# Performance work log

Measured on AMD Instinct MI355X. Metric: run time of the kernel, lower is better.

## Reference

```python
import jax, jax.numpy as jnp
import numpy as np

B = 524288   # batch
I = 12       # input_props
R = 6        # output_props (rules)
J = 2        # templates per rule
L = 2        # feature width
V = 4        # variables


def setup_inputs() -> dict:
    key = jax.random.key(0)
    ks = jax.random.split(key, 7)
    concrete_features = jax.random.uniform(ks[0], (B, I, L), dtype=jnp.float32)
    templates = jax.random.uniform(ks[1], (R, J, L), dtype=jnp.float32)           # U(0,1)
    gammas = jax.random.uniform(ks[2], (R, J, L), dtype=jnp.float32) * 0.4 + 0.4  # U(0.4,0.8)
    body_W = jax.random.normal(ks[3], (R, J, V, L), dtype=jnp.float32) * 0.5
    body_b = jax.random.normal(ks[4], (R, J, V), dtype=jnp.float32) * 0.1
    head_W = jax.random.normal(ks[5], (R, L, V), dtype=jnp.float32) * 0.5
    head_b = jax.random.normal(ks[6], (R, L), dtype=jnp.float32) * 0.1
    return {"concrete_features": concrete_features, "templates": templates,
            "gammas": gammas, "body_W": body_W, "body_b": body_b,
            "head_W": head_W, "head_b": head_b}


def reference(concrete_features, templates, gammas, body_W, body_b, head_W, head_b):
    # "sigmoid" in the original is clamp(x, 0, 1)
    g = jnp.clip(gammas, 0.0, 1.0)            # [R,J,L]
    w = 1.0 - g                               # per-dim match weight
    # match_scores[b,r,j,i] = sum_l w[r,j,l] * (templates[r,j,l] - f[b,i,l])^2
    # expand the square to avoid materializing a [B,R,J,I,L] tensor
    c0 = jnp.sum(w * templates * templates, axis=-1)                       # [R,J]
    cross = jnp.einsum('rjl,bil->brji', w * templates, concrete_features)  # [B,R,J,I]
    quad = jnp.einsum('rjl,bil->brji', w, concrete_features ** 2)          # [B,R,J,I]
    match_scores = c0[None, :, :, None] - 2.0 * cross + quad               # [B,R,J,I]
    attn = jax.nn.softmax(-match_scores, axis=-1)                          # over input_props
    # soft-selected feature per (rule, template): [B,R,J,L]
    selected = jnp.einsum('brji,bil->brjl', attn, concrete_features)
    # body Linear per (r,j), then sum over j (biases also sum over j)
    captured = jnp.einsum('brjl,rjvl->brv', selected, body_W) + jnp.sum(body_b, axis=1)  # [B,R,V]
    # head Linear per rule
    out = jnp.einsum('brv,rlv->brl', captured, head_W) + head_b            # [B,R,L]
    return out
```

## Files before the change

### kernel.cpp

```cpp
#include <hip/hip_runtime.h>

#define NI 12
#define NR 6
#define NJ 2
#define NL 2
#define NV 4

typedef float v2f __attribute__((ext_vector_type(2)));


__global__ __launch_bounds__(256) void
abstraction_fused(const float* __restrict__ feat,
                  const float* __restrict__ templates,
                  const float* __restrict__ gammas,
                  const float* __restrict__ body_W,
                  const float* __restrict__ body_b,
                  const float* __restrict__ head_W,
                  const float* __restrict__ head_b,
                  float* __restrict__ out, int B) {
    __shared__ float sG[NR * NJ * 5];
    __shared__ float sM[NR * NL * NJ * NL];
    __shared__ float sC[NR * NL];

    const int t = threadIdx.x;
    const float LOG2E = 1.4426950408889634f;

    if (t < NR * NJ) {
        const int g = t;
        float g0 = fminf(fmaxf(gammas[g * NL + 0], 0.f), 1.f);
        float g1 = fminf(fmaxf(gammas[g * NL + 1], 0.f), 1.f);
        float w0 = 1.f - g0, w1 = 1.f - g1;
        float t0 = templates[g * NL + 0], t1 = templates[g * NL + 1];
        float wt0 = w0 * t0, wt1 = w1 * t1;
        float c0 = wt0 * t0 + wt1 * t1;
        sG[g * 5 + 0] = 2.f * LOG2E * wt0;
        sG[g * 5 + 1] = 2.f * LOG2E * wt1;
        sG[g * 5 + 2] = -LOG2E * w0;
        sG[g * 5 + 3] = -LOG2E * w1;
        sG[g * 5 + 4] = -LOG2E * c0;
    } else if (t >= 64 && t < 64 + NR * NL) {
        const int idx = t - 64;
        const int r = idx >> 1, l = idx & 1;
        float acc = head_b[r * NL + l];
        #pragma unroll
        for (int v = 0; v < NV; ++v) {
            float bs = body_b[(r * NJ + 0) * NV + v] + body_b[(r * NJ + 1) * NV + v];
            acc = fmaf(head_W[(r * NL + l) * NV + v], bs, acc);
        }
        sC[idx] = acc;
    } else if (t >= 128 && t < 128 + NR * NL * NJ * NL) {
        const int idx = t - 128;
        const int lp = idx & 1, j = (idx >> 1) & 1, l = (idx >> 2) & 1, r = idx >> 3;
        float acc = 0.f;
        #pragma unroll
        for (int v = 0; v < NV; ++v)
            acc = fmaf(head_W[(r * NL + l) * NV + v],
                       body_W[((r * NJ + j) * NV + v) * NL + lp], acc);
        sM[idx] = acc;
    }
    __syncthreads();

    const int b = blockIdx.x * blockDim.x + t;
    if (b >= B) return;

    const float4* fp = (const float4*)(feat + (size_t)b * (NI * NL));
    float f0[NI], f1[NI];
    #pragma unroll
    for (int k = 0; k < 6; ++k) {
        float4 v = fp[k];
        f0[2 * k + 0] = v.x; f1[2 * k + 0] = v.y;
        f0[2 * k + 1] = v.z; f1[2 * k + 1] = v.w;
    }

    float o[NR * NL];
    #pragma unroll
    for (int r = 0; r < NR; ++r) {
        float o0 = sC[r * 2 + 0];
        float o1 = sC[r * 2 + 1];
        #pragma unroll
        for (int j = 0; j < NJ; ++j) {
            const int g = r * NJ + j;
            const v2f A0 = sG[g * 5 + 0];
            const v2f A1 = sG[g * 5 + 1];
            const v2f W0 = sG[g * 5 + 2];
            const v2f W1 = sG[g * 5 + 3];
            const v2f Cn = sG[g * 5 + 4];
            v2f den = 0.f, a0 = 0.f, a1 = 0.f;
            #pragma unroll
            for (int i = 0; i < NI; i += 2) {
                v2f X0 = { f0[i], f0[i + 1] };
                v2f X1 = { f1[i], f1[i + 1] };
                v2f n = __builtin_elementwise_fma(X0, __builtin_elementwise_fma(W0, X0, A0), Cn);
                n = __builtin_elementwise_fma(X1, __builtin_elementwise_fma(W1, X1, A1), n);
                v2f p = { __builtin_amdgcn_exp2f(n.x), __builtin_amdgcn_exp2f(n.y) };
                den += p;
                a0 = __builtin_elementwise_fma(p, X0, a0);
                a1 = __builtin_elementwise_fma(p, X1, a1);
            }
            float d = den.x + den.y;
            float rinv = __builtin_amdgcn_rcpf(d);
            float s0 = (a0.x + a0.y) * rinv;
            float s1 = (a1.x + a1.y) * rinv;
            const float m00 = sM[((r * 2 + 0) * 2 + j) * 2 + 0];
            const float m01 = sM[((r * 2 + 0) * 2 + j) * 2 + 1];
            const float m10 = sM[((r * 2 + 1) * 2 + j) * 2 + 0];
            const float m11 = sM[((r * 2 + 1) * 2 + j) * 2 + 1];
            o0 = fmaf(s0, m00, o0); o0 = fmaf(s1, m01, o0);
            o1 = fmaf(s0, m10, o1); o1 = fmaf(s1, m11, o1);
        }
        o[r * 2 + 0] = o0;
        o[r * 2 + 1] = o1;
    }

    float4* op = (float4*)(out + (size_t)b * (NR * NL));
    op[0] = make_float4(o[0], o[1], o[2], o[3]);
    op[1] = make_float4(o[4], o[5], o[6], o[7]);
    op[2] = make_float4(o[8], o[9], o[10], o[11]);
}

extern "C" void kernel_launch(void* const* d_in, const int* in_sizes, int n_in,
                              void* d_out, int out_size, void* d_ws, size_t ws_size,
                              hipStream_t stream) {
    (void)n_in; (void)out_size; (void)d_ws; (void)ws_size;
    const float* feat      = (const float*)d_in[0];
    const float* templates = (const float*)d_in[1];
    const float* gammas    = (const float*)d_in[2];
    const float* body_W    = (const float*)d_in[3];
    const float* body_b    = (const float*)d_in[4];
    const float* head_W    = (const float*)d_in[5];
    const float* head_b    = (const float*)d_in[6];
    float* out = (float*)d_out;

    int B = in_sizes[0] / (NI * NL);
    int blocks = (B + 255) / 256;
    hipLaunchKernelGGL(abstraction_fused, dim3(blocks), dim3(256), 0, stream,
                       feat, templates, gammas, body_W, body_b, head_W, head_b,
                       out, B);
}
```

Measured before the change: 107.7 us.

## Split parameter precompute into separate kernel reading constants from workspace

Moves the per-block parameter folding (templates/gammas/body/head weights) into a one-block precompute kernel that writes a packed record into the workspace. The main kernel then reads these uniform values straight from global memory, likely as scalar loads, with no shared memory and no __syncthreads. This removes redundant per-block setup work and the block-wide barrier. The cost is a second kernel launch and a dependency between the two kernels.

```diff
diff --git a/kernel.cpp b/kernel.cpp
--- a/kernel.cpp
+++ b/kernel.cpp
@@ -8,59 +8,63 @@
 
 typedef float v2f __attribute__((ext_vector_type(2)));
 
+#define LOG2E 1.4426950408889634f
 
-__global__ __launch_bounds__(256) void
-abstraction_fused(const float* __restrict__ feat,
-                  const float* __restrict__ templates,
-                  const float* __restrict__ gammas,
-                  const float* __restrict__ body_W,
-                  const float* __restrict__ body_b,
-                  const float* __restrict__ head_W,
-                  const float* __restrict__ head_b,
-                  float* __restrict__ out, int B) {
-    __shared__ float sG[NR * NJ * 5];
-    __shared__ float sM[NR * NL * NJ * NL];
-    __shared__ float sC[NR * NL];
 
+__global__ __launch_bounds__(64) void
+abstraction_params(const float* __restrict__ templates,
+                   const float* __restrict__ gammas,
+                   const float* __restrict__ body_W,
+                   const float* __restrict__ body_b,
+                   const float* __restrict__ head_W,
+                   const float* __restrict__ head_b,
+                   float* __restrict__ P) {
     const int t = threadIdx.x;
-    const float LOG2E = 1.4426950408889634f;
-
     if (t < NR * NJ) {
-        const int g = t;
+        const int g = t, r = g >> 1, j = g & 1;
         float g0 = fminf(fmaxf(gammas[g * NL + 0], 0.f), 1.f);
         float g1 = fminf(fmaxf(gammas[g * NL + 1], 0.f), 1.f);
         float w0 = 1.f - g0, w1 = 1.f - g1;
         float t0 = templates[g * NL + 0], t1 = templates[g * NL + 1];
-        float wt0 = w0 * t0, wt1 = w1 * t1;
-        float c0 = wt0 * t0 + wt1 * t1;
-        sG[g * 5 + 0] = 2.f * LOG2E * wt0;
-        sG[g * 5 + 1] = 2.f * LOG2E * wt1;
-        sG[g * 5 + 2] = -LOG2E * w0;
-        sG[g * 5 + 3] = -LOG2E * w1;
-        sG[g * 5 + 4] = -LOG2E * c0;
-    } else if (t >= 64 && t < 64 + NR * NL) {
-        const int idx = t - 64;
-        const int r = idx >> 1, l = idx & 1;
+        float A0 = 2.f * LOG2E * w0 * t0, A1 = 2.f * LOG2E * w1 * t1;
+        float W0 = -LOG2E * w0, W1 = -LOG2E * w1;
+        float Cn = -LOG2E * (w0 * t0 * t0 + w1 * t1 * t1);
+        float* rec = P + g * 16;
+        rec[0] = A0; rec[1] = A0;
+        rec[2] = A1; rec[3] = A1;
+        rec[4] = W0; rec[5] = W0;
+        rec[6] = W1; rec[7] = W1;
+        rec[8] = Cn; rec[9] = Cn;
+        #pragma unroll
+        for (int l = 0; l < NL; ++l) {
+            #pragma unroll
+            for (int lp = 0; lp < NL; ++lp) {
+                float acc = 0.f;
+                #pragma unroll
+                for (int v = 0; v < NV; ++v)
+                    acc = fmaf(head_W[(r * NL + l) * NV + v],
+                               body_W[((r * NJ + j) * NV + v) * NL + lp], acc);
+                rec[10 + l * 2 + lp] = acc;
+            }
+        }
+        rec[14] = 0.f; rec[15] = 0.f;
+    } else if (t >= 32 && t < 32 + NR * NL) {
+        const int idx = t - 32, r = idx >> 1, l = idx & 1;
         float acc = head_b[r * NL + l];
-        #pragma unroll
-        for (int v = 0; v < NV; ++v) {
-            float bs = body_b[(r * NJ + 0) * NV + v] + body_b[(r * NJ + 1) * NV + v];
-            acc = fmaf(head_W[(r * NL + l) * NV + v], bs, acc);
-        }
-        sC[idx] = acc;
-    } else if (t >= 128 && t < 128 + NR * NL * NJ * NL) {
-        const int idx = t - 128;
-        const int lp = idx & 1, j = (idx >> 1) & 1, l = (idx >> 2) & 1, r = idx >> 3;
-        float acc = 0.f;
         #pragma unroll
         for (int v = 0; v < NV; ++v)
             acc = fmaf(head_W[(r * NL + l) * NV + v],
-                       body_W[((r * NJ + j) * NV + v) * NL + lp], acc);
-        sM[idx] = acc;
+                       body_b[(r * NJ + 0) * NV + v] + body_b[(r * NJ + 1) * NV + v],
+                       acc);
+        P[192 + idx] = acc;
     }
-    __syncthreads();
+}
 
-    const int b = blockIdx.x * blockDim.x + t;
+__global__ __launch_bounds__(256) void
+abstraction_main(const float* __restrict__ feat,
+                 const float* __restrict__ P,
+                 float* __restrict__ out, int B) {
+    const int b = blockIdx.x * 256 + threadIdx.x;
     if (b >= B) return;
 
     const float4* fp = (const float4*)(feat + (size_t)b * (NI * NL));
@@ -75,16 +79,16 @@
     float o[NR * NL];
     #pragma unroll
     for (int r = 0; r < NR; ++r) {
-        float o0 = sC[r * 2 + 0];
-        float o1 = sC[r * 2 + 1];
+        float o0 = P[192 + r * 2 + 0];
+        float o1 = P[192 + r * 2 + 1];
         #pragma unroll
         for (int j = 0; j < NJ; ++j) {
-            const int g = r * NJ + j;
-            const v2f A0 = sG[g * 5 + 0];
-            const v2f A1 = sG[g * 5 + 1];
-            const v2f W0 = sG[g * 5 + 2];
-            const v2f W1 = sG[g * 5 + 3];
-            const v2f Cn = sG[g * 5 + 4];
+            const float* __restrict__ rec = P + (r * NJ + j) * 16;
+            const v2f A0 = *(const v2f*)(rec + 0);
+            const v2f A1 = *(const v2f*)(rec + 2);
+            const v2f W0 = *(const v2f*)(rec + 4);
+            const v2f W1 = *(const v2f*)(rec + 6);
+            const v2f Cn = *(const v2f*)(rec + 8);
             v2f den = 0.f, a0 = 0.f, a1 = 0.f;
             #pragma unroll
             for (int i = 0; i < NI; i += 2) {
@@ -101,12 +105,8 @@
             float rinv = __builtin_amdgcn_rcpf(d);
             float s0 = (a0.x + a0.y) * rinv;
             float s1 = (a1.x + a1.y) * rinv;
-            const float m00 = sM[((r * 2 + 0) * 2 + j) * 2 + 0];
-            const float m01 = sM[((r * 2 + 0) * 2 + j) * 2 + 1];
-            const float m10 = sM[((r * 2 + 1) * 2 + j) * 2 + 0];
-            const float m11 = sM[((r * 2 + 1) * 2 + j) * 2 + 1];
-            o0 = fmaf(s0, m00, o0); o0 = fmaf(s1, m01, o0);
-            o1 = fmaf(s0, m10, o1); o1 = fmaf(s1, m11, o1);
+            o0 = fmaf(s0, rec[10], o0); o0 = fmaf(s1, rec[11], o0);
+            o1 = fmaf(s0, rec[12], o1); o1 = fmaf(s1, rec[13], o1);
         }
         o[r * 2 + 0] = o0;
         o[r * 2 + 1] = o1;
@@ -121,7 +121,7 @@
 extern "C" void kernel_launch(void* const* d_in, const int* in_sizes, int n_in,
                               void* d_out, int out_size, void* d_ws, size_t ws_size,
                               hipStream_t stream) {
-    (void)n_in; (void)out_size; (void)d_ws; (void)ws_size;
+    (void)n_in; (void)out_size; (void)ws_size;
     const float* feat      = (const float*)d_in[0];
     const float* templates = (const float*)d_in[1];
     const float* gammas    = (const float*)d_in[2];
@@ -130,10 +130,13 @@
     const float* head_W    = (const float*)d_in[5];
     const float* head_b    = (const float*)d_in[6];
     float* out = (float*)d_out;
+    float* P   = (float*)d_ws;
 
     int B = in_sizes[0] / (NI * NL);
     int blocks = (B + 255) / 256;
-    hipLaunchKernelGGL(abstraction_fused, dim3(blocks), dim3(256), 0, stream,
-                       feat, templates, gammas, body_W, body_b, head_W, head_b,
-                       out, B);
+
+    hipLaunchKernelGGL(abstraction_params, dim3(1), dim3(64), 0, stream,
+                       templates, gammas, body_W, body_b, head_W, head_b, P);
+    hipLaunchKernelGGL(abstraction_main, dim3(blocks), dim3(256), 0, stream,
+                       feat, P, out, B);
 }
```

New measurement: 110.0 us. +2.2%, slower.
